# Kernel tuning notes

Hardware: AMD Instinct MI355X
Metric: run time of the kernel (lower is better)

## Reference

```python
import jax, jax.numpy as jnp
import numpy as np

N_TOKENS = 131072
N_E = 1024
E_DIM = 256
BETA = 0.25
GAMMA = 0.99


def setup_inputs() -> dict:
    key = jax.random.key(0)
    k1, k2 = jax.random.split(key)
    z = jax.random.normal(k1, (N_TOKENS, E_DIM), dtype=jnp.float32)
    # nn.Embedding weight init: uniform(-1/n_e, 1/n_e)
    emb_weight = jax.random.uniform(k2, (N_E, E_DIM), dtype=jnp.float32,
                                    minval=-1.0 / N_E, maxval=1.0 / N_E)
    n_mat = jnp.ones((1, N_E), dtype=jnp.float32)
    m_mat = jnp.ones((N_E, E_DIM), dtype=jnp.float32)
    return {"z": z, "emb_weight": emb_weight, "n_mat": n_mat, "m_mat": m_mat,
            "batch_size": 128, "n_train": 100000}


def reference(z, emb_weight, n_mat, m_mat, batch_size, n_train):
    n_e, e_dim = emb_weight.shape
    zf = z.reshape(-1, e_dim)  # (N, e_dim)

    # squared-distance matrix: ||z||^2 + ||e||^2 - 2 z e^T  -> (N, n_e)
    d = (jnp.sum(zf * zf, axis=1, keepdims=True)
         + jnp.sum(emb_weight * emb_weight, axis=1)
         - 2.0 * (zf @ emb_weight.T))
    idx = jnp.argmin(d, axis=1)                       # (N,)
    min_encodings = jax.nn.one_hot(idx, n_e, dtype=z.dtype)  # (N, n_e)

    # z_q = one_hot @ weight == gather
    z_q = emb_weight[idx].reshape(z.shape)

    # EMA codebook update (the Python per-codeword loop == segment reductions)
    counts = jnp.sum(min_encodings, axis=0)           # (n_e,)
    new_n_mat = n_mat * GAMMA + counts[None, :] * (1.0 - GAMMA)
    sums = jax.ops.segment_sum(zf, idx, num_segments=n_e)  # (n_e, e_dim)
    new_m_mat = GAMMA * m_mat + (1.0 - GAMMA) * sums
    new_emb_weight = new_m_mat / new_n_mat[0][:, None]

    commit_loss = BETA * jnp.mean((jax.lax.stop_gradient(z_q) - z) ** 2)
    quant_loss = jnp.mean((z_q - jax.lax.stop_gradient(z)) ** 2)
    z_q_st = z + jax.lax.stop_gradient(z_q - z)       # straight-through

    e_mean = counts / zf.shape[0]
    perplexity = jnp.exp(-jnp.sum(e_mean * jnp.log(e_mean + 1e-10)))

    return (quant_loss, commit_loss, z_q_st, perplexity, min_encodings,
            idx[:, None], new_emb_weight, new_n_mat, new_m_mat)
```

## Files before the change

### kernel.cpp

```cpp
#include <hip/hip_runtime.h>


#define NT 131072
#define NE 1024
#define ED 256

typedef _Float16 f16;
typedef f16  f16x8 __attribute__((ext_vector_type(8)));
typedef float f32x4 __attribute__((ext_vector_type(4)));

static const size_t OFF_QL   = 0;
static const size_t OFF_CL   = 1;
static const size_t OFF_ZQ   = 2;
static const size_t OFF_PPL  = 33554434ULL;
static const size_t OFF_OH   = 33554435ULL;
static const size_t OFF_IDX  = 167772163ULL;
static const size_t OFF_NEMB = 167903235ULL;
static const size_t OFF_NN   = 168165379ULL;
static const size_t OFF_NM   = 168166403ULL;

__global__ __launch_bounds__(256) void rownorm_k(const float* __restrict__ x,
                                                 float* __restrict__ o, int nrows) {
  int wid  = blockIdx.x * 4 + (threadIdx.x >> 6);
  int lane = threadIdx.x & 63;
  if (wid >= nrows) return;
  float4 v = ((const float4*)(x + (size_t)wid * ED))[lane];
  float s = v.x * v.x + v.y * v.y + v.z * v.z + v.w * v.w;
  #pragma unroll
  for (int off = 32; off; off >>= 1) s += __shfl_down(s, off, 64);
  if (lane == 0) o[wid] = s;
}

__global__ __launch_bounds__(256) void eprep_k(const float* __restrict__ emb,
                                               char* __restrict__ eswz) {
  const int t  = threadIdx.x;
  const int c  = blockIdx.x * 8 + (t >> 5);
  const int kq = t & 31;
  const float* er = emb + (size_t)c * ED + kq * 8;
  float4 v0 = ((const float4*)er)[0];
  float4 v1 = ((const float4*)er)[1];
  float vv[8] = {v0.x, v0.y, v0.z, v0.w, v1.x, v1.y, v1.z, v1.w};
  f16x8 h;
  #pragma unroll
  for (int i = 0; i < 8; ++i) h[i] = (f16)(vv[i] * 1024.0f);
  const int tile = c >> 5, cl = c & 31;
  const int g = (cl << 5) | (kq ^ (cl & 7));
  *(f16x8*)(eswz + (size_t)tile * 16384 + (size_t)g * 16) = h;
}

__global__ __launch_bounds__(256) void argmin_coarse_k(
    const float* __restrict__ z, const char* __restrict__ eswz,
    const float* __restrict__ enorm, int* __restrict__ idxw,
    int* __restrict__ nflag, int* __restrict__ flaglist) {
  const int tid  = threadIdx.x;
  const int w    = tid >> 6, lane = tid & 63;
  const int lr   = lane & 15, kg = lane >> 4;
  const int r0   = blockIdx.x * 128 + w * 32;

  f16x8 ah[2][8];
  #pragma unroll
  for (int mf = 0; mf < 2; ++mf) {
    const float* zr = z + (size_t)(r0 + mf * 16 + lr) * ED + kg * 8;
    #pragma unroll
    for (int kt = 0; kt < 8; ++kt) {
      float4 a = ((const float4*)(zr + kt * 32))[0];
      float4 b = ((const float4*)(zr + kt * 32))[1];
      float vv[8] = {a.x, a.y, a.z, a.w, b.x, b.y, b.z, b.w};
      #pragma unroll
      for (int i = 0; i < 8; ++i) ah[mf][kt][i] = (f16)vv[i];
    }
  }

  const int xr = lr & 7;
  int boff[8];
  #pragma unroll
  for (int kt = 0; kt < 8; ++kt)
    boff[kt] = lr * 512 + (((kt * 4 + kg) ^ xr) << 4);

  float m1[2][4], m2[2][4]; int i1[2][4];
  #pragma unroll
  for (int mf = 0; mf < 2; ++mf)
    #pragma unroll
    for (int r = 0; r < 4; ++r) {
      m1[mf][r] = 3.4028235e38f; m2[mf][r] = 3.4028235e38f; i1[mf][r] = 0;
    }

  for (int ct = 0; ct < 32; ++ct) {
    const char* tb = eswz + (size_t)ct * 16384;

    f32x4 acc[2][2];
    #pragma unroll
    for (int mf = 0; mf < 2; ++mf)
      #pragma unroll
      for (int nf = 0; nf < 2; ++nf) acc[mf][nf] = (f32x4){0.f, 0.f, 0.f, 0.f};

    #pragma unroll
    for (int kt = 0; kt < 8; ++kt) {
      f16x8 b0, b1;
      __builtin_memcpy(&b0, tb + boff[kt], 16);
      __builtin_memcpy(&b1, tb + boff[kt] + 8192, 16);
      acc[0][0] = __builtin_amdgcn_mfma_f32_16x16x32_f16(ah[0][kt], b0, acc[0][0], 0, 0, 0);
      acc[1][0] = __builtin_amdgcn_mfma_f32_16x16x32_f16(ah[1][kt], b0, acc[1][0], 0, 0, 0);
      acc[0][1] = __builtin_amdgcn_mfma_f32_16x16x32_f16(ah[0][kt], b1, acc[0][1], 0, 0, 0);
      acc[1][1] = __builtin_amdgcn_mfma_f32_16x16x32_f16(ah[1][kt], b1, acc[1][1], 0, 0, 0);
    }

    #pragma unroll
    for (int nf = 0; nf < 2; ++nf) {
      const int c = ct * 32 + nf * 16 + lr;
      const float en = enorm[c];
      #pragma unroll
      for (int mf = 0; mf < 2; ++mf)
        #pragma unroll
        for (int r = 0; r < 4; ++r) {
          float dd = en - 0.001953125f * acc[mf][nf][r];
          if (dd < m1[mf][r]) {
            m2[mf][r] = m1[mf][r]; m1[mf][r] = dd; i1[mf][r] = c;
          } else if (dd < m2[mf][r]) {
            m2[mf][r] = dd;
          }
        }
    }
  }

  #pragma unroll
  for (int mf = 0; mf < 2; ++mf)
    #pragma unroll
    for (int r = 0; r < 4; ++r) {
      float a1 = m1[mf][r]; int ai = i1[mf][r]; float a2 = m2[mf][r];
      #pragma unroll
      for (int off = 1; off < 16; off <<= 1) {
        float o1 = __shfl_xor(a1, off, 64);
        int   oi = __shfl_xor(ai, off, 64);
        float o2 = __shfl_xor(a2, off, 64);
        if (o1 < a1) { a2 = fminf(a1, o2); a1 = o1; ai = oi; }
        else         { a2 = fminf(a2, o1); }
      }
      if (lr == 0) {
        const int row = r0 + mf * 16 + kg * 4 + r;
        idxw[row] = ai;
        if (a2 - a1 < 4.0e-4f) {
          int p = atomicAdd(nflag, 1);
          flaglist[p] = row;
        }
      }
    }
}

__global__ __launch_bounds__(256) void argmin_refine_k(
    const float* __restrict__ z, const float* __restrict__ emb,
    const float* __restrict__ znorm, const float* __restrict__ enorm,
    const int* __restrict__ nflag, const int* __restrict__ flaglist,
    int* __restrict__ idxw) {
  const int nf = *nflag;
  const int b0 = blockIdx.x * 16;
  if (b0 >= nf) return;

  __shared__ float zl[16][256];
  __shared__ int   toks[16];
  __shared__ float rv[4][16];
  __shared__ int   ri[4][16];

  const int t = threadIdx.x;
  if (t < 16) {
    int li = b0 + t;
    toks[t] = flaglist[li < nf ? li : b0];
  }
  __syncthreads();

  #pragma unroll
  for (int i = 0; i < 4; ++i) {
    int li = t + i * 256;
    int row = li >> 6, c4 = li & 63;
    float4 v = ((const float4*)(z + (size_t)toks[row] * ED))[c4];
    *(float4*)&zl[row][c4 * 4] = v;
  }
  __syncthreads();

  float acc[4][16];
  #pragma unroll
  for (int cc = 0; cc < 4; ++cc)
    #pragma unroll
    for (int tk = 0; tk < 16; ++tk) acc[cc][tk] = 0.f;

  for (int c4 = 0; c4 < 64; ++c4) {
    float4 e[4];
    #pragma unroll
    for (int cc = 0; cc < 4; ++cc)
      e[cc] = ((const float4*)(emb + (size_t)(t * 4 + cc) * ED))[c4];
    #pragma unroll
    for (int tk = 0; tk < 16; ++tk) {
      float4 zv = *(const float4*)&zl[tk][c4 * 4];
      #pragma unroll
      for (int cc = 0; cc < 4; ++cc) {
        acc[cc][tk] += zv.x * e[cc].x;
        acc[cc][tk] += zv.y * e[cc].y;
        acc[cc][tk] += zv.z * e[cc].z;
        acc[cc][tk] += zv.w * e[cc].w;
      }
    }
  }

  float en[4];
  #pragma unroll
  for (int cc = 0; cc < 4; ++cc) en[cc] = enorm[t * 4 + cc];

  const int wv = t >> 6, lane = t & 63;
  for (int tk = 0; tk < 16; ++tk) {
    const float zn = znorm[toks[tk]];
    float bv = 3.4028235e38f; int bi = 0;
    #pragma unroll
    for (int cc = 0; cc < 4; ++cc) {
      float s = zn + en[cc];
      float d = s - 2.0f * acc[cc][tk];
      int   c = t * 4 + cc;
      if (d < bv) { bv = d; bi = c; }
    }
    #pragma unroll
    for (int off = 32; off; off >>= 1) {
      float ov = __shfl_down(bv, off, 64);
      int   oi = __shfl_down(bi, off, 64);
      if (ov < bv || (ov == bv && oi < bi)) { bv = ov; bi = oi; }
    }
    if (lane == 0) { rv[wv][tk] = bv; ri[wv][tk] = bi; }
  }
  __syncthreads();
  if (t < 16) {
    float bv = rv[0][t]; int bi = ri[0][t];
    #pragma unroll
    for (int wq = 1; wq < 4; ++wq) {
      float ov = rv[wq][t]; int oi = ri[wq][t];
      if (ov < bv || (ov == bv && oi < bi)) { bv = ov; bi = oi; }
    }
    idxw[toks[t]] = bi;
  }
}

__global__ __launch_bounds__(256) void zq_oh_k(
    const float* __restrict__ z, const float* __restrict__ emb,
    const int* __restrict__ idxw, float* __restrict__ out,
    double* __restrict__ lossacc) {
  const int t = threadIdx.x;
  const int tl = t >> 6, lane = t & 63;
  const int tok = blockIdx.x * 4 + tl;
  const int id = idxw[tok];

  float4 z4 = ((const float4*)(z   + (size_t)tok * ED))[lane];
  float4 e4 = ((const float4*)(emb + (size_t)id  * ED))[lane];
  float4 q;
  q.x = z4.x + (e4.x - z4.x);
  q.y = z4.y + (e4.y - z4.y);
  q.z = z4.z + (e4.z - z4.z);
  q.w = z4.w + (e4.w - z4.w);
  __builtin_memcpy(out + OFF_ZQ + (size_t)tok * ED + (size_t)lane * 4, &q, 16);

  float dx = e4.x - z4.x, dy = e4.y - z4.y, dz = e4.z - z4.z, dw = e4.w - z4.w;
  double lsum = (double)(dx * dx) + (double)(dy * dy)
              + (double)(dz * dz) + (double)(dw * dw);

  float* ohb = out + OFF_OH + (size_t)tok * NE;
  #pragma unroll
  for (int it = 0; it < 4; ++it) {
    int f4i = it * 64 + lane;
    int c0 = f4i * 4;
    float v[4];
    v[0] = (c0 + 0 == id) ? 1.0f : 0.0f;
    v[1] = (c0 + 1 == id) ? 1.0f : 0.0f;
    v[2] = (c0 + 2 == id) ? 1.0f : 0.0f;
    v[3] = (c0 + 3 == id) ? 1.0f : 0.0f;
    __builtin_memcpy(ohb + (size_t)f4i * 4, v, 16);
  }

  #pragma unroll
  for (int off = 32; off; off >>= 1) lsum += __shfl_down(lsum, off, 64);
  __shared__ double lred[4];
  if (lane == 0) lred[tl] = lsum;
  __syncthreads();
  if (t == 0)
    unsafeAtomicAdd(&lossacc[blockIdx.x & 255],
                    lred[0] + lred[1] + lred[2] + lred[3]);
}

__global__ __launch_bounds__(256) void hist_k(const int* __restrict__ idxw,
                                              int* __restrict__ counts) {
  __shared__ int lc[NE];
  for (int i = threadIdx.x; i < NE; i += 256) lc[i] = 0;
  __syncthreads();
  const int stride = gridDim.x * 256;
  for (int i = blockIdx.x * 256 + threadIdx.x; i < NT; i += stride)
    atomicAdd(&lc[idxw[i]], 1);
  __syncthreads();
  for (int i = threadIdx.x; i < NE; i += 256) {
    int v = lc[i];
    if (v) atomicAdd(&counts[i], v);
  }
}

__global__ __launch_bounds__(256) void scan_k(const int* __restrict__ counts,
                                              int* __restrict__ offsets) {
  const int t = threadIdx.x;
  const int lane = t & 63, w = t >> 6;
  int4 c = ((const int4*)counts)[t];
  int s = c.x + c.y + c.z + c.w;
  int v = s;
  #pragma unroll
  for (int off = 1; off < 64; off <<= 1) {
    int u = __shfl_up(v, off, 64);
    if (lane >= off) v += u;
  }
  __shared__ int wsum[4];
  if (lane == 63) wsum[w] = v;
  __syncthreads();
  int base = 0;
  #pragma unroll
  for (int i = 0; i < 4; ++i) if (i < w) base += wsum[i];
  int excl = base + v - s;
  int4 o;
  o.x = excl;
  o.y = o.x + c.x;
  o.z = o.y + c.y;
  o.w = o.z + c.z;
  ((int4*)offsets)[t] = o;
}

__global__ __launch_bounds__(256) void scatter_k(
    const int* __restrict__ idxw, const int* __restrict__ offsets,
    int* __restrict__ cursor, int* __restrict__ bucket,
    float* __restrict__ out) {
  int i = blockIdx.x * 256 + threadIdx.x;
  int id = idxw[i];
  out[OFF_IDX + i] = (float)id;
  int pos = atomicAdd(&cursor[id], 1);
  bucket[offsets[id] + pos] = i;
}

__global__ __launch_bounds__(256) void segsum_k(
    const float* __restrict__ z, const float* __restrict__ nmat,
    const float* __restrict__ mmat, const int* __restrict__ counts,
    const int* __restrict__ offsets, const int* __restrict__ bucket,
    float* __restrict__ out) {
  const int j = blockIdx.x, t = threadIdx.x;
  const int cnt = counts[j], off = offsets[j];
  float s = 0.f;
  int i = 0;
  for (; i + 4 <= cnt; i += 4) {
    int t0 = bucket[off + i + 0], t1 = bucket[off + i + 1];
    int t2 = bucket[off + i + 2], t3 = bucket[off + i + 3];
    float a = z[(size_t)t0 * ED + t];
    float b = z[(size_t)t1 * ED + t];
    float c = z[(size_t)t2 * ED + t];
    float d = z[(size_t)t3 * ED + t];
    s += a; s += b; s += c; s += d;
  }
  for (; i < cnt; ++i) s += z[(size_t)bucket[off + i] * ED + t];

  float newn = nmat[j] * 0.99f + (float)cnt * 0.01f;
  if (t == 0) out[OFF_NN + j] = newn;
  const size_t o = (size_t)j * ED + t;
  float newm = 0.99f * mmat[o] + 0.01f * s;
  out[OFF_NM + o]   = newm;
  out[OFF_NEMB + o] = newm / newn;
}

__global__ __launch_bounds__(256) void scalars_k(
    const double* __restrict__ lossacc, const int* __restrict__ counts,
    float* __restrict__ out) {
  const int t = threadIdx.x;
  double lsum = lossacc[t];
  double h = 0.0;
  for (int c = t; c < NE; c += 256) {
    double e = (double)counts[c] / (double)NT;
    h += e * log(e + 1e-10);
  }
  #pragma unroll
  for (int off = 32; off; off >>= 1) {
    lsum += __shfl_down(lsum, off, 64);
    h    += __shfl_down(h,    off, 64);
  }
  __shared__ double sl[4], sh[4];
  if ((t & 63) == 0) { sl[t >> 6] = lsum; sh[t >> 6] = h; }
  __syncthreads();
  if (t == 0) {
    double mean = (sl[0] + sl[1] + sl[2] + sl[3]) / (double)((size_t)NT * ED);
    out[OFF_QL]  = (float)mean;
    out[OFF_CL]  = (float)(0.25 * mean);
    out[OFF_PPL] = (float)exp(-(sh[0] + sh[1] + sh[2] + sh[3]));
  }
}

extern "C" void kernel_launch(void* const* d_in, const int* in_sizes, int n_in,
                              void* d_out, int out_size, void* d_ws, size_t ws_size,
                              hipStream_t stream) {
  const float* z    = (const float*)d_in[0];
  const float* emb  = (const float*)d_in[1];
  const float* nmat = (const float*)d_in[2];
  const float* mmat = (const float*)d_in[3];
  float* out = (float*)d_out;
  char*  ws  = (char*)d_ws;

  double* lossacc = (double*)ws;
  int*    nflag   = (int*)(ws + 2048);
  int*    counts  = (int*)(ws + 4096);
  int*    cursor  = (int*)(ws + 8192);
  int*    offsets = (int*)(ws + 12288);
  int*    bucket  = (int*)(ws + 16384);
  int*    idxw    = (int*)(ws + 540672);
  float*  znorm   = (float*)(ws + 1064960);
  float*  enorm   = (float*)(ws + 1589248);
  char*   eswz    = ws + 1593344;
  int*    flaglist= (int*)(ws + 2117632);

  hipMemsetAsync(ws, 0, 12288, stream);

  hipLaunchKernelGGL(rownorm_k, dim3(NT / 4), dim3(256), 0, stream, z, znorm, NT);
  hipLaunchKernelGGL(rownorm_k, dim3(NE / 4), dim3(256), 0, stream, emb, enorm, NE);
  hipLaunchKernelGGL(eprep_k, dim3(NE / 8), dim3(256), 0, stream, emb, eswz);
  hipLaunchKernelGGL(argmin_coarse_k, dim3(NT / 128), dim3(256), 0, stream,
                     z, eswz, enorm, idxw, nflag, flaglist);
  hipLaunchKernelGGL(argmin_refine_k, dim3(NT / 16), dim3(256), 0, stream,
                     z, emb, znorm, enorm, nflag, flaglist, idxw);
  hipLaunchKernelGGL(zq_oh_k, dim3(NT / 4), dim3(256), 0, stream,
                     z, emb, idxw, out, lossacc);
  hipLaunchKernelGGL(hist_k, dim3(64), dim3(256), 0, stream, idxw, counts);
  hipLaunchKernelGGL(scan_k, dim3(1), dim3(256), 0, stream, counts, offsets);
  hipLaunchKernelGGL(scatter_k, dim3(NT / 256), dim3(256), 0, stream,
                     idxw, offsets, cursor, bucket, out);
  hipLaunchKernelGGL(segsum_k, dim3(NE), dim3(256), 0, stream,
                     z, nmat, mmat, counts, offsets, bucket, out);
  hipLaunchKernelGGL(scalars_k, dim3(1), dim3(256), 0, stream,
                     lossacc, counts, out);
}
```

Baseline: 1.403 ms.

## Double-buffer codebook tiles in LDS via async global-to-LDS loads in argmin kernel

```diff
diff --git a/kernel.cpp b/kernel.cpp
--- a/kernel.cpp
+++ b/kernel.cpp
@@ -18,6 +18,12 @@
 static const size_t OFF_NEMB = 167903235ULL;
 static const size_t OFF_NN   = 168165379ULL;
 static const size_t OFF_NM   = 168166403ULL;
+
+__device__ __forceinline__ void gload_lds16(const void* g, void* l) {
+  __builtin_amdgcn_global_load_lds(
+      (const __attribute__((address_space(1))) unsigned int*)g,
+      (__attribute__((address_space(3))) unsigned int*)l, 16, 0, 0);
+}
 
 __global__ __launch_bounds__(256) void rownorm_k(const float* __restrict__ x,
                                                  float* __restrict__ o, int nrows) {
@@ -48,10 +54,12 @@
   *(f16x8*)(eswz + (size_t)tile * 16384 + (size_t)g * 16) = h;
 }
 
-__global__ __launch_bounds__(256) void argmin_coarse_k(
+__global__ __launch_bounds__(256, 2) void argmin_coarse_k(
     const float* __restrict__ z, const char* __restrict__ eswz,
     const float* __restrict__ enorm, int* __restrict__ idxw,
     int* __restrict__ nflag, int* __restrict__ flaglist) {
+  __shared__ uint4 ebuf[2][1024];
+
   const int tid  = threadIdx.x;
   const int w    = tid >> 6, lane = tid & 63;
   const int lr   = lane & 15, kg = lane >> 4;
@@ -71,12 +79,6 @@
     }
   }
 
-  const int xr = lr & 7;
-  int boff[8];
-  #pragma unroll
-  for (int kt = 0; kt < 8; ++kt)
-    boff[kt] = lr * 512 + (((kt * 4 + kg) ^ xr) << 4);
-
   float m1[2][4], m2[2][4]; int i1[2][4];
   #pragma unroll
   for (int mf = 0; mf < 2; ++mf)
@@ -85,8 +87,23 @@
       m1[mf][r] = 3.4028235e38f; m2[mf][r] = 3.4028235e38f; i1[mf][r] = 0;
     }
 
+  const int soff = w * 4096 + lane * 16;
+  #pragma unroll
+  for (int c = 0; c < 4; ++c)
+    gload_lds16(eswz + soff + c * 1024,
+                (char*)ebuf[0] + w * 4096 + c * 1024);
+  __syncthreads();
+
   for (int ct = 0; ct < 32; ++ct) {
-    const char* tb = eswz + (size_t)ct * 16384;
+    const int cur = ct & 1;
+    if (ct < 31) {
+      const char* ntb = eswz + (size_t)(ct + 1) * 16384 + soff;
+      #pragma unroll
+      for (int c = 0; c < 4; ++c)
+        gload_lds16(ntb + c * 1024,
+                    (char*)ebuf[cur ^ 1] + w * 4096 + c * 1024);
+    }
+    const char* eb = (const char*)ebuf[cur];
 
     f32x4 acc[2][2];
     #pragma unroll
@@ -97,8 +114,14 @@
     #pragma unroll
     for (int kt = 0; kt < 8; ++kt) {
       f16x8 b0, b1;
-      __builtin_memcpy(&b0, tb + boff[kt], 16);
-      __builtin_memcpy(&b1, tb + boff[kt] + 8192, 16);
+      #pragma unroll
+      for (int nf = 0; nf < 2; ++nf) {
+        const int cl = nf * 16 + lr;
+        const int kq = kt * 4 + kg;
+        const int u  = (cl << 5) | (kq ^ (cl & 7));
+        f16x8 bv = *(const f16x8*)(eb + u * 16);
+        if (nf == 0) b0 = bv; else b1 = bv;
+      }
       acc[0][0] = __builtin_amdgcn_mfma_f32_16x16x32_f16(ah[0][kt], b0, acc[0][0], 0, 0, 0);
       acc[1][0] = __builtin_amdgcn_mfma_f32_16x16x32_f16(ah[1][kt], b0, acc[1][0], 0, 0, 0);
       acc[0][1] = __builtin_amdgcn_mfma_f32_16x16x32_f16(ah[0][kt], b1, acc[0][1], 0, 0, 0);
@@ -121,6 +144,7 @@
           }
         }
     }
+    __syncthreads();
   }
 
   #pragma unroll
```

After: 1.259 ms. 10.3% less time.
